# Optimization experiments

Hardware: AMD Instinct MI355X
Metric: run time of the kernel (lower is better)

## Reference

```python
import jax, jax.numpy as jnp
import numpy as np
from jax import lax

SR = 16000
N_FFT = 400
HOP = 200
N_MELS = 128
HID = 128


def _mel_fb():
    # torchaudio melscale_fbanks defaults: htk scale, norm=None, f_min=0, f_max=sr/2
    all_freqs = np.linspace(0.0, SR / 2, N_FFT // 2 + 1)  # (201,)
    hz2mel = lambda f: 2595.0 * np.log10(1.0 + f / 700.0)
    mel2hz = lambda m: 700.0 * (10.0 ** (m / 2595.0) - 1.0)
    m_pts = np.linspace(hz2mel(0.0), hz2mel(SR / 2), N_MELS + 2)
    f_pts = mel2hz(m_pts)  # (130,)
    f_diff = np.diff(f_pts)  # (129,)
    slopes = f_pts[None, :] - all_freqs[:, None]  # (201,130)
    down = -slopes[:, :-2] / f_diff[:-1]
    up = slopes[:, 2:] / f_diff[1:]
    fb = np.maximum(0.0, np.minimum(down, up))  # (201,128)
    return jnp.asarray(fb, dtype=jnp.float32)

MEL_FB = _mel_fb()
HANN = jnp.asarray(np.hanning(N_FFT + 1)[:-1], dtype=jnp.float32)  # periodic hann(400)


def mel_spectrogram(x):
    # x: (B, T) waveform -> (B, n_mels, frames), power=2 mel spectrogram
    pad = N_FFT // 2
    xp = jnp.pad(x, ((0, 0), (pad, pad)), mode='reflect')
    n_frames = 1 + (xp.shape[1] - N_FFT) // HOP  # 81 for T=16000
    idx = jnp.arange(n_frames)[:, None] * HOP + jnp.arange(N_FFT)[None, :]
    frames = xp[:, idx] * HANN  # (B, frames, 400)
    spec = jnp.fft.rfft(frames, axis=-1)  # (B, frames, 201)
    power = jnp.abs(spec) ** 2
    mel = power @ MEL_FB  # (B, frames, 128)
    return jnp.transpose(mel, (0, 2, 1))  # (B, 128, frames)


def lstm_layer(x, W, U, b):
    # x: (B, T, F); gate order i, f, g, o (matches torch slicing)
    B = x.shape[0]
    h0 = jnp.zeros((B, HID), x.dtype)
    c0 = jnp.zeros((B, HID), x.dtype)

    def step(carry, x_t):
        h, c = carry
        gates = x_t @ W + h @ U + b  # (B, 4H)
        i = jax.nn.sigmoid(gates[:, :HID])
        f = jax.nn.sigmoid(gates[:, HID:2 * HID])
        g = jnp.tanh(gates[:, 2 * HID:3 * HID])
        o = jax.nn.sigmoid(gates[:, 3 * HID:])
        c = f * c + i * g
        h = o * jnp.tanh(c)
        return (h, c), h

    _, hs = lax.scan(step, (h0, c0), jnp.transpose(x, (1, 0, 2)))  # (T, B, H)
    return jnp.transpose(hs, (1, 0, 2))  # (B, T, H)


def setup_inputs() -> dict:
    key = jax.random.key(0)
    ks = jax.random.split(key, 16)
    s = 0.05
    return {
        'x': jax.random.normal(ks[0], (1024, 16000), dtype=jnp.float32),
        'conv_w': jax.random.normal(ks[1], (128, 128, 3), dtype=jnp.float32) * s,  # (out,in,k)
        'conv_b': jax.random.normal(ks[2], (128,), dtype=jnp.float32) * s,
        'W1': jax.random.normal(ks[3], (128, 4 * HID), dtype=jnp.float32) * s,
        'U1': jax.random.normal(ks[4], (HID, 4 * HID), dtype=jnp.float32) * s,
        'b1': jax.random.normal(ks[5], (4 * HID,), dtype=jnp.float32) * s,
        'W2': jax.random.normal(ks[6], (HID, 4 * HID), dtype=jnp.float32) * s,
        'U2': jax.random.normal(ks[7], (HID, 4 * HID), dtype=jnp.float32) * s,
        'b2': jax.random.normal(ks[8], (4 * HID,), dtype=jnp.float32) * s,
        'fc1_w': jax.random.normal(ks[9], (128, 128), dtype=jnp.float32) * s,  # (in,out)
        'fc1_b': jax.random.normal(ks[10], (128,), dtype=jnp.float32) * s,
        'proj_w': jax.random.normal(ks[11], (128, 35), dtype=jnp.float32) * s,  # (in,out)
        'proj_b': jax.random.normal(ks[12], (35,), dtype=jnp.float32) * s,
    }


def reference(x, conv_w, conv_b, W1, U1, b1, W2, U2, b2, fc1_w, fc1_b, proj_w, proj_b):
    # MelSpectrogram -> Conv1d(128,128,3) -> permute -> LSTM x2 -> fc1 -> mean(time) -> proj
    spec = mel_spectrogram(x)  # (B, 128, 81)
    conv = lax.conv_general_dilated(
        spec, conv_w, window_strides=(1,), padding='VALID',
        dimension_numbers=('NCH', 'OIH', 'NCH')) + conv_b[None, :, None]  # (B,128,79)
    h = jnp.transpose(conv, (0, 2, 1))  # (B, 79, 128)
    h = lstm_layer(h, W1, U1, b1)
    h = lstm_layer(h, W2, U2, b2)
    h = h @ fc1_w + fc1_b  # (B, 79, 128)
    h = jnp.mean(h, axis=1)  # (B, 128)
    return h @ proj_w + proj_b  # (B, 35)
```

## Files before the change

kernel.cpp:

```cpp
#include <hip/hip_runtime.h>
#include <math.h>

#define PI_D 3.14159265358979323846

#define BATCH   1024
#define TLEN    16000
#define NFFT    400
#define HOP     200
#define NFRAME  81
#define NBIN    201
#define NMEL    128
#define HID     128
#define TSTEPS  79
#define GATES   512

#define KDFT    416
#define NDFT    512
#define SINOFF  256
#define KPOW    224
#define KCONV   384
#define NCHUNK  2
#define CHROWS  (BATCH*NFRAME/NCHUNK)

static inline size_t al512(size_t v){ return (v + 511) & ~((size_t)511); }

__device__ __forceinline__ unsigned short bf_rne(float f){
    unsigned u = __float_as_uint(f);
    u += 0x7FFF + ((u >> 16) & 1);
    return (unsigned short)(u >> 16);
}
__device__ __forceinline__ void bf_split(float f, unsigned short& h, unsigned short& l){
    h = bf_rne(f);
    float hf = __uint_as_float(((unsigned)h) << 16);
    l = bf_rne(f - hf);
}
__device__ __forceinline__ void bf_split_fast(float f, unsigned short& h, unsigned short& l){
    unsigned u = __float_as_uint(f);
    h = (unsigned short)(u >> 16);
    float hf = __uint_as_float(u & 0xFFFF0000u);
    l = (unsigned short)(__float_as_uint(f - hf) >> 16);
}

__device__ __forceinline__ int kswz(int n, int k){
    return (k & ~31) | (((((k >> 3) & 3) ^ ((n >> 1) & 3))) << 3) | (k & 7);
}

typedef short bf16x8 __attribute__((ext_vector_type(8)));
typedef float f32x4  __attribute__((ext_vector_type(4)));
typedef unsigned short us8 __attribute__((ext_vector_type(8)));
typedef unsigned short us4 __attribute__((ext_vector_type(4)));
typedef _Float16 f16x8 __attribute__((ext_vector_type(8)));

__device__ __forceinline__ void gld16(const unsigned short* g, unsigned short* l){
    __builtin_amdgcn_global_load_lds(
        (const __attribute__((address_space(1))) unsigned int*)g,
        (__attribute__((address_space(3))) unsigned int*)l, 16, 0, 0);
}

__global__ void setup_dft_t(unsigned short* __restrict__ th, unsigned short* __restrict__ tl){
    int idx = blockIdx.x*256 + threadIdx.x;
    if (idx >= NDFT*KDFT) return;
    int n = idx / KDFT, k = idx % KDFT;
    double v = 0.0;
    if (k < 400) {
        double w = 0.5 - 0.5*cos(2.0*PI_D*(double)k/400.0);
        if (n < NBIN)                              v = w * cos(2.0*PI_D*(double)((k*n)%400)/400.0);
        else if (n >= SINOFF && n < SINOFF + NBIN) v = w * sin(2.0*PI_D*(double)((k*(n-SINOFF))%400)/400.0);
    }
    unsigned short h, l; bf_split((float)v, h, l);
    int o = n*KDFT + kswz(n, k);
    th[o] = h; tl[o] = l;
}

__global__ void setup_fb_t(unsigned short* __restrict__ fh, unsigned short* __restrict__ fl){
    int idx = blockIdx.x*256 + threadIdx.x;
    if (idx >= NMEL*KPOW) return;
    int m = idx / KPOW, f = idx % KPOW;
    float v = 0.f;
    if (f < NBIN) {
        double melmax = 2595.0 * log10(1.0 + 8000.0/700.0);
        double p0 = 700.0*(pow(10.0, melmax*(double)(m  )/129.0/2595.0) - 1.0);
        double p1 = 700.0*(pow(10.0, melmax*(double)(m+1)/129.0/2595.0) - 1.0);
        double p2 = 700.0*(pow(10.0, melmax*(double)(m+2)/129.0/2595.0) - 1.0);
        double freq = 40.0 * (double)f;
        double dn = (freq - p0)/(p1 - p0);
        double up = (p2 - freq)/(p2 - p1);
        double t  = dn < up ? dn : up;
        if (t < 0.0) t = 0.0;
        v = (float)t;
    }
    unsigned short h, l; bf_split(v, h, l);
    int o = m*KPOW + kswz(m, f);
    fh[o] = h; fl[o] = l;
}

__global__ void setup_wc_t(unsigned short* __restrict__ wh, unsigned short* __restrict__ wl,
                           const float* __restrict__ cw){
    int idx = blockIdx.x*256 + threadIdx.x;
    if (idx >= NMEL*KCONV) return;
    int o = idx / KCONV, kk = idx % KCONV;
    int ksh = kk >> 7, i = kk & 127;
    unsigned short h, l; bf_split(cw[o*384 + i*3 + ksh], h, l);
    int p = o*KCONV + kswz(o, kk);
    wh[p] = h; wl[p] = l;
}

__global__ void setup_w_t(unsigned short* __restrict__ wh, unsigned short* __restrict__ wl,
                          const float* __restrict__ w){
    int idx = blockIdx.x*256 + threadIdx.x;
    if (idx >= GATES*HID) return;
    int c = idx / HID, i = idx % HID;
    unsigned short h, l; bf_split(w[(size_t)i*GATES + c], h, l);
    int p = c*HID + kswz(c, i);
    wh[p] = h; wl[p] = l;
}

__global__ void setup_comb(float* __restrict__ cwm, float* __restrict__ cb,
                           const float* __restrict__ fc1w, const float* __restrict__ fc1b,
                           const float* __restrict__ projw, const float* __restrict__ projb){
    int idx = blockIdx.x*256 + threadIdx.x;
    if (idx < 128*64) {
        int i = idx / 64, o = idx % 64;
        float v = 0.f;
        if (o < 35) {
            double s = 0.0;
            for (int m = 0; m < 128; m++) s += (double)fc1w[i*128+m] * (double)projw[m*35+o];
            v = (float)s;
        }
        cwm[idx] = v;
    } else if (idx < 128*64 + 64) {
        int o = idx - 128*64;
        float v = 0.f;
        if (o < 35) {
            double s = (double)projb[o];
            for (int m = 0; m < 128; m++) s += (double)fc1b[m] * (double)projw[m*35+o];
            v = (float)s;
        }
        cb[o] = v;
    }
}

__global__ void setup_uf(_Float16* __restrict__ uf, const float* __restrict__ u){
    int idx = blockIdx.x*256 + threadIdx.x;
    if (idx >= 65536) return;
    int j    = idx & 7;
    int lane = (idx >> 3) & 63;
    int nt   = (idx >> 9) & 3;
    int ks   = (idx >> 11) & 3;
    int w    = (idx >> 13) & 7;
    int k = ks*32 + (lane >> 4)*8 + j;
    int c = w*64 + nt*16 + (lane & 15);
    uf[idx] = (_Float16)u[(size_t)k*GATES + c];
}

enum AMode { A_NORMAL=0, A_FRAMES=1, A_POWER=2, A_CONV3=3 };

template<int AMODE, bool BIAS, int NT, bool WIDE>
__global__ __launch_bounds__(256)
void mgemm_k(const float* __restrict__ A,
             const unsigned short* __restrict__ BTh, const unsigned short* __restrict__ BTl,
             const float* __restrict__ bias, float* __restrict__ C,
             int Ksteps, int lda, int kstride, int ldc,
             const float* __restrict__ aux, int rowbase)
{
    constexpr int BM = WIDE ? 64 : 128;
    constexpr int BN = WIDE ? 256 : 128;
    constexpr int AP = BM / 32;
    __shared__ unsigned short Ash[2][BM][32], Asl[2][BM][32];
    __shared__ unsigned short Bsh[2][BN][32], Bsl[2][BN][32];

    const int nwg = gridDim.x;
    const int qq = nwg >> 3, rmd = nwg & 7;
    const int xcd = blockIdx.x & 7, loc = blockIdx.x >> 3;
    const int swz = (xcd < rmd ? xcd*(qq+1) : rmd*(qq+1) + (xcd - rmd)*qq) + loc;
    constexpr int LGNT = (NT == 4) ? 2 : (NT == 2) ? 1 : 0;
    const int m0 = (swz >> LGNT) * BM;
    const int n0 = (swz & (NT-1)) * BN;

    const int tid = threadIdx.x;
    const int lane = tid & 63, w = tid >> 6;
    const int wr = WIDE ? 0 : (w >> 1) * 64;
    const int wc = WIDE ? w * 64 : (w & 1) * 64;
    const int l15 = lane & 15;
    const int swf = ((lane & 15) >> 1) & 3;
    const int pos = (((lane >> 4) ^ swf) << 3);

    const int sr  = tid >> 3;
    const int wcol = (((((tid & 7) >> 1)) ^ ((tid >> 4) & 3)) << 3) + ((tid & 1) << 2);

    float va0[AP*4], vb0[AP*4], va1[AP*4], vb1[AP*4];

    auto issue_loads = [&](float (&va)[AP*4], float (&vb)[AP*4], int ksn){
        const int k0n = ksn * 32;
        #pragma unroll
        for (int p = 0; p < AP; p++) {
            const int row = p*32 + sr;
            const int kk = k0n + (tid & 7)*4;
            if constexpr (AMODE == A_NORMAL) {
                *(float4*)&va[p*4] = *(const float4*)(A + (size_t)(m0+row)*lda + kk);
            } else if constexpr (AMODE == A_POWER) {
                const float* src = A + (size_t)(m0+row)*lda + kk;
                *(float4*)&va[p*4] = *(const float4*)(src);
                *(float4*)&vb[p*4] = *(const float4*)(src + SINOFF);
            } else if constexpr (AMODE == A_FRAMES) {
                const int rr = rowbase + m0 + row;
                const int b = rr / NFRAME, f = rr - b*NFRAME;
                const float* xb = aux + (size_t)b * TLEN;
                const int q0 = f*HOP + kk - 200;
                if (q0 >= 0 && q0 + 3 < TLEN) {
                    *(float4*)&va[p*4] = *(const float4*)(xb + q0);
                } else {
                    #pragma unroll
                    for (int j = 0; j < 4; j++) {
                        int q = q0 + j;
                        if (q < 0) q = -q;
                        else if (q >= TLEN) q = 2*TLEN - 2 - q;
                        va[p*4+j] = xb[q];
                    }
                }
            } else {
                const int rr = m0 + row;
                const int b = rr / TSTEPS, t = rr - b*TSTEPS;
                const int ksh = kk >> 7, i = kk & 127;
                *(float4*)&va[p*4] = *(const float4*)(aux + ((size_t)(b*NFRAME + t + ksh)*NMEL + i));
            }
        }
        (void)vb;
    };
    auto write_stage = [&](float (&va)[AP*4], float (&vb)[AP*4], int wb){
        #pragma unroll
        for (int p = 0; p < AP; p++) {
            const int row = p*32 + sr;
            us4 hv, lv;
            #pragma unroll
            for (int j = 0; j < 4; j++) {
                float f = va[p*4+j];
                if constexpr (AMODE == A_POWER) f = f*f + vb[p*4+j]*vb[p*4+j];
                unsigned short h, l; bf_split_fast(f, h, l);
                hv[j] = h; lv[j] = l;
            }
            *(us4*)&Ash[wb][row][wcol] = hv;
            *(us4*)&Asl[wb][row][wcol] = lv;
        }
        (void)vb;
    };
    auto dma_b = [&](int wb, int ksn){
        const int k0n = ksn * 32;
        if constexpr (WIDE) {
            #pragma unroll
            for (int p = 0; p < 4; p++) {
                const int row = w*64 + p*16;
                const size_t o = (size_t)(n0 + row + (lane >> 2))*kstride + k0n + (lane & 3)*8;
                gld16(BTh + o, &Bsh[wb][row][0]);
                gld16(BTl + o, &Bsl[wb][row][0]);
            }
        } else {
            #pragma unroll
            for (int p = 0; p < 2; p++) {
                const int row = p*64 + w*16;
                const size_t o = (size_t)(n0 + row + (lane >> 2))*kstride + k0n + (lane & 3)*8;
                gld16(BTh + o, &Bsh[wb][row][0]);
                gld16(BTl + o, &Bsl[wb][row][0]);
            }
        }
    };

    f32x4 acc[4][4] = {};

    issue_loads(va1, vb1, 0);
    dma_b(0, 0);
    write_stage(va1, vb1, 0);
    issue_loads(va0, vb0, 1);
    __syncthreads();

    auto iter = [&](int ks, float (&vac)[AP*4], float (&vbc)[AP*4],
                    float (&vao)[AP*4], float (&vbo)[AP*4], int bufc){
        const bool pf1 = (ks + 1 < Ksteps);
        const bool pf2 = (ks + 2 < Ksteps);
        if (pf2) issue_loads(vao, vbo, ks + 2);
        if (pf1) dma_b(bufc ^ 1, ks + 1);

        bf16x8 ah[4], al[4];
        #pragma unroll
        for (int mt = 0; mt < 4; mt++) {
            ah[mt] = *(const bf16x8*)&Ash[bufc][wr + mt*16 + l15][pos];
            al[mt] = *(const bf16x8*)&Asl[bufc][wr + mt*16 + l15][pos];
        }
        #pragma unroll
        for (int nt = 0; nt < 4; nt++) {
            const int nr = wc + nt*16 + l15;
            bf16x8 bh = *(const bf16x8*)&Bsh[bufc][nr][pos];
            bf16x8 bl = *(const bf16x8*)&Bsl[bufc][nr][pos];
            #pragma unroll
            for (int mt = 0; mt < 4; mt++) {
                acc[mt][nt] = __builtin_amdgcn_mfma_f32_16x16x32_bf16(ah[mt], bh, acc[mt][nt], 0, 0, 0);
                acc[mt][nt] = __builtin_amdgcn_mfma_f32_16x16x32_bf16(ah[mt], bl, acc[mt][nt], 0, 0, 0);
                acc[mt][nt] = __builtin_amdgcn_mfma_f32_16x16x32_bf16(al[mt], bh, acc[mt][nt], 0, 0, 0);
            }
        }

        if (pf1) {
            write_stage(vac, vbc, bufc ^ 1);
            __syncthreads();
        }
    };

    for (int ks = 0; ks < Ksteps; ks += 2) {
        iter(ks, va0, vb0, va1, vb1, 0);
        if (ks + 1 < Ksteps) iter(ks + 1, va1, vb1, va0, vb0, 1);
    }

    const int quad = lane >> 4;
    #pragma unroll
    for (int nt = 0; nt < 4; nt++) {
        const int col = n0 + wc + (nt << 4) + l15;
        float b = 0.f;
        if constexpr (BIAS) b = bias[col];
        #pragma unroll
        for (int mt = 0; mt < 4; mt++) {
            #pragma unroll
            for (int r = 0; r < 4; r++) {
                const int row = m0 + wr + (mt << 4) + quad*4 + r;
                C[(size_t)row*ldc + col] = acc[mt][nt][r] + b;
            }
        }
    }
}

__global__ __launch_bounds__(256)
void gemm_small(const float* __restrict__ A, const float* __restrict__ Bm,
                const float* __restrict__ bias, float* __restrict__ C,
                int M, int N, int K, int lda, int ldb, int ldc)
{
    __shared__ float As[16][64+4];
    __shared__ float Bs[16][64];
    const int tid = threadIdx.x;
    const int tx = tid & 15, ty = tid >> 4;
    const int m0 = blockIdx.x * 64;
    float acc[4][4] = {{0,0,0,0},{0,0,0,0},{0,0,0,0},{0,0,0,0}};
    const int am = tid >> 2, ak = (tid & 3) * 4;
    const int bk = tid >> 4, bn = (tid & 15) * 4;
    for (int k0 = 0; k0 < K; k0 += 16) {
        float4 av = *(const float4*)(A + (size_t)(m0+am)*lda + k0 + ak);
        As[ak+0][am]=av.x; As[ak+1][am]=av.y; As[ak+2][am]=av.z; As[ak+3][am]=av.w;
        *(float4*)&Bs[bk][bn] = *(const float4*)(Bm + (size_t)(k0+bk)*ldb + bn);
        __syncthreads();
        #pragma unroll
        for (int k = 0; k < 16; k++) {
            float4 a = *(const float4*)&As[k][ty*4];
            float4 b = *(const float4*)&Bs[k][tx*4];
            #pragma unroll
            for (int i = 0; i < 4; i++) {
                float av_ = ((const float*)&a)[i];
                acc[i][0] = fmaf(av_, b.x, acc[i][0]);
                acc[i][1] = fmaf(av_, b.y, acc[i][1]);
                acc[i][2] = fmaf(av_, b.z, acc[i][2]);
                acc[i][3] = fmaf(av_, b.w, acc[i][3]);
            }
        }
        __syncthreads();
    }
    #pragma unroll
    for (int ir = 0; ir < 4; ir++) {
        const int row = m0 + ty*4 + ir;
        #pragma unroll
        for (int jc = 0; jc < 4; jc++) {
            const int col = tx*4 + jc;
            if (col < N) C[(size_t)row*ldc + col] = acc[ir][jc] + bias[col];
        }
    }
}

__device__ __forceinline__ float sigm_f(float x){ return 1.f/(1.f + __expf(-x)); }
__device__ __forceinline__ float tanh_f(float x){ float e = __expf(2.f*x); return 1.f - 2.f/(e + 1.f); }

#define LROWS 4
#define LTHREADS 512
#define HPAD 136

__global__ __launch_bounds__(LTHREADS, 2)
void lstm_k(const float* __restrict__ X, const _Float16* __restrict__ Uf, float* __restrict__ H)
{
    __shared__ _Float16 hsA[16*HPAD];
    __shared__ float gs[GATES*5];
    const int tid = threadIdx.x;
    const int b0 = blockIdx.x * LROWS;
    const int lane = tid & 63, w = tid >> 6;
    const int m16 = lane & 15, quad = lane >> 4;
    const int r = tid >> 7;
    const int j = tid & 127;

    f32x4 bfr[4][4];
    #pragma unroll
    for (int ks = 0; ks < 4; ks++)
        #pragma unroll
        for (int nt = 0; nt < 4; nt++) {
            bfr[ks][nt] = *(const f32x4*)(Uf + ((((w*4 + ks)*4 + nt)*64 + lane) << 3));
            asm volatile("" : "+v"(bfr[ks][nt]));
        }

    for (int i = tid; i < 16*HPAD; i += LTHREADS) hsA[i] = (_Float16)0.f;
    float cst = 0.f;
    const float* xb = X + ((size_t)(b0 + r)*TSTEPS)*GATES + j;
    __syncthreads();

    float xi = xb[0], xf = xb[128], xg = xb[256], xo = xb[384];

    for (int t = 0; t < TSTEPS; t++) {
        float xi_n = 0.f, xf_n = 0.f, xg_n = 0.f, xo_n = 0.f;
        if (t + 1 < TSTEPS) {
            const float* xp = xb + (size_t)(t + 1)*GATES;
            xi_n = xp[0]; xf_n = xp[128]; xg_n = xp[256]; xo_n = xp[384];
        }

        f16x8 ah[4];
        #pragma unroll
        for (int ks = 0; ks < 4; ks++)
            ah[ks] = *(const f16x8*)&hsA[m16*HPAD + ks*32 + quad*8];

        f32x4 acc[4] = {{0,0,0,0},{0,0,0,0},{0,0,0,0},{0,0,0,0}};
        #pragma unroll
        for (int ks = 0; ks < 4; ks++)
            #pragma unroll
            for (int nt = 0; nt < 4; nt++)
                acc[nt] = __builtin_amdgcn_mfma_f32_16x16x32_f16(
                    ah[ks], __builtin_bit_cast(f16x8, bfr[ks][nt]), acc[nt], 0, 0, 0);

        if (quad == 0) {
            #pragma unroll
            for (int nt = 0; nt < 4; nt++) {
                const int c = w*64 + nt*16 + m16;
                #pragma unroll
                for (int rr = 0; rr < 4; rr++) gs[c*5 + rr] = acc[nt][rr];
            }
        }
        __syncthreads();

        {
            const float gi = gs[(      j)*5 + r] + xi;
            const float gf = gs[(128 + j)*5 + r] + xf;
            const float gg = gs[(256 + j)*5 + r] + xg;
            const float go = gs[(384 + j)*5 + r] + xo;
            const float cn = sigm_f(gf)*cst + sigm_f(gi)*tanh_f(gg);
            cst = cn;
            const float hn = sigm_f(go)*tanh_f(cn);
            H[((size_t)(b0 + r)*TSTEPS + t)*HID + j] = hn;
            hsA[r*HPAD + j] = (_Float16)hn;
        }
        __syncthreads();

        xi = xi_n; xf = xf_n; xg = xg_n; xo = xo_n;
    }
}

__global__ void mean_k(const float* __restrict__ H, float* __restrict__ Mh){
    const int idx = blockIdx.x*256 + threadIdx.x;
    if (idx >= BATCH*HID) return;
    const int b = idx >> 7, j = idx & 127;
    const float* p = H + (size_t)b*TSTEPS*HID + j;
    float s = 0.f;
    for (int t = 0; t < TSTEPS; t++) s += p[(size_t)t*HID];
    Mh[idx] = s * (1.0f/(float)TSTEPS);
}

extern "C" void kernel_launch(void* const* d_in, const int* in_sizes, int n_in,
                              void* d_out, int out_size, void* d_ws, size_t ws_size,
                              hipStream_t stream)
{
    const float* x      = (const float*)d_in[0];
    const float* conv_w = (const float*)d_in[1];
    const float* conv_b = (const float*)d_in[2];
    const float* W1     = (const float*)d_in[3];
    const float* U1     = (const float*)d_in[4];
    const float* b1     = (const float*)d_in[5];
    const float* W2     = (const float*)d_in[6];
    const float* U2     = (const float*)d_in[7];
    const float* b2     = (const float*)d_in[8];
    const float* fc1_w  = (const float*)d_in[9];
    const float* fc1_b  = (const float*)d_in[10];
    const float* proj_w = (const float*)d_in[11];
    const float* proj_b = (const float*)d_in[12];
    float* out = (float*)d_out;

    char* ws = (char*)d_ws;
    size_t off = 0;
    unsigned short* Tth = (unsigned short*)(ws + off); off = al512(off + (size_t)NDFT*KDFT*2);
    unsigned short* Ttl = (unsigned short*)(ws + off); off = al512(off + (size_t)NDFT*KDFT*2);
    unsigned short* fbh = (unsigned short*)(ws + off); off = al512(off + (size_t)NMEL*KPOW*2);
    unsigned short* fbl = (unsigned short*)(ws + off); off = al512(off + (size_t)NMEL*KPOW*2);
    unsigned short* wch = (unsigned short*)(ws + off); off = al512(off + (size_t)NMEL*KCONV*2);
    unsigned short* wcl = (unsigned short*)(ws + off); off = al512(off + (size_t)NMEL*KCONV*2);
    unsigned short* w1h = (unsigned short*)(ws + off); off = al512(off + (size_t)GATES*HID*2);
    unsigned short* w1l = (unsigned short*)(ws + off); off = al512(off + (size_t)GATES*HID*2);
    unsigned short* w2h = (unsigned short*)(ws + off); off = al512(off + (size_t)GATES*HID*2);
    unsigned short* w2l = (unsigned short*)(ws + off); off = al512(off + (size_t)GATES*HID*2);
    float* Cw   = (float*)(ws + off); off = al512(off + (size_t)128*64*4);
    float* Cb   = (float*)(ws + off); off = al512(off + (size_t)64*4);
    float* Mh   = (float*)(ws + off); off = al512(off + (size_t)BATCH*HID*4);
    _Float16* Uf1 = (_Float16*)(ws + off); off = al512(off + (size_t)65536*2);
    _Float16* Uf2 = (_Float16*)(ws + off); off = al512(off + (size_t)65536*2);
    float* MEL  = (float*)(ws + off); off = al512(off + (size_t)BATCH*NFRAME*NMEL*4);
    float* CONV = (float*)(ws + off); off = al512(off + (size_t)BATCH*TSTEPS*NMEL*4);
    float* X    = (float*)(ws + off); off = al512(off + (size_t)BATCH*TSTEPS*GATES*4);
    float* DFT = X;
    float* H1  = MEL;
    float* H2  = CONV;
    (void)ws_size; (void)out_size; (void)n_in; (void)in_sizes;

    setup_dft_t<<<(NDFT*KDFT + 255)/256, 256, 0, stream>>>(Tth, Ttl);
    setup_fb_t <<<(NMEL*KPOW + 255)/256, 256, 0, stream>>>(fbh, fbl);
    setup_wc_t <<<(NMEL*KCONV + 255)/256, 256, 0, stream>>>(wch, wcl, conv_w);
    setup_w_t  <<<(GATES*HID + 255)/256, 256, 0, stream>>>(w1h, w1l, W1);
    setup_w_t  <<<(GATES*HID + 255)/256, 256, 0, stream>>>(w2h, w2l, W2);
    setup_comb <<<(128*64 + 64 + 255)/256, 256, 0, stream>>>(Cw, Cb, fc1_w, fc1_b, proj_w, proj_b);
    setup_uf   <<<65536/256, 256, 0, stream>>>(Uf1, U1);
    setup_uf   <<<65536/256, 256, 0, stream>>>(Uf2, U2);

    for (int ch = 0; ch < NCHUNK; ch++) {
        const int rowbase = ch * CHROWS;
        mgemm_k<A_FRAMES,false,2,true><<<(CHROWS/64)*2, 256, 0, stream>>>(
            nullptr, Tth, Ttl, nullptr, DFT, KDFT/32, 0, KDFT, NDFT, x, rowbase);
        mgemm_k<A_POWER,false,1,false><<<CHROWS/128, 256, 0, stream>>>(
            DFT, fbh, fbl, nullptr, MEL + (size_t)rowbase*NMEL, KPOW/32, NDFT, KPOW, NMEL, nullptr, 0);
    }

    mgemm_k<A_CONV3,true,1,false><<<BATCH*TSTEPS/128, 256, 0, stream>>>(
        nullptr, wch, wcl, conv_b, CONV, KCONV/32, 0, KCONV, NMEL, MEL, 0);

    mgemm_k<A_NORMAL,true,2,true><<<(BATCH*TSTEPS/64)*2, 256, 0, stream>>>(
        CONV, w1h, w1l, b1, X, HID/32, NMEL, HID, GATES, nullptr, 0);
    lstm_k<<<BATCH/LROWS, LTHREADS, 0, stream>>>(X, Uf1, H1);

    mgemm_k<A_NORMAL,true,2,true><<<(BATCH*TSTEPS/64)*2, 256, 0, stream>>>(
        H1, w2h, w2l, b2, X, HID/32, HID, HID, GATES, nullptr, 0);
    lstm_k<<<BATCH/LROWS, LTHREADS, 0, stream>>>(X, Uf2, H2);

    mean_k<<<(BATCH*HID + 255)/256, 256, 0, stream>>>(H2, Mh);
    gemm_small<<<BATCH/64, 256, 0, stream>>>(Mh, Cw, Cb, out, BATCH, 35, HID, HID, 64, 35);
}
```

Measured before the change: 666.1 us.

## Replace LSTM step barriers with LDS-only waits, spread gate writes, deepen prefetch

```diff
diff --git a/kernel.cpp b/kernel.cpp
--- a/kernel.cpp
+++ b/kernel.cpp
@@ -55,6 +55,13 @@
     __builtin_amdgcn_global_load_lds(
         (const __attribute__((address_space(1))) unsigned int*)g,
         (__attribute__((address_space(3))) unsigned int*)l, 16, 0, 0);
+}
+
+__device__ __forceinline__ void barrier_lds(){
+    __builtin_amdgcn_sched_barrier(0);
+    asm volatile("s_waitcnt lgkmcnt(0)" ::: "memory");
+    __builtin_amdgcn_s_barrier();
+    __builtin_amdgcn_sched_barrier(0);
 }
 
 __global__ void setup_dft_t(unsigned short* __restrict__ th, unsigned short* __restrict__ tl){
@@ -404,13 +411,14 @@
     const float* xb = X + ((size_t)(b0 + r)*TSTEPS)*GATES + j;
     __syncthreads();
 
-    float xi = xb[0], xf = xb[128], xg = xb[256], xo = xb[384];
+    float xi  = xb[0],     xf  = xb[128],     xg  = xb[256],     xo  = xb[384];
+    float xi1 = xb[GATES], xf1 = xb[GATES+128], xg1 = xb[GATES+256], xo1 = xb[GATES+384];
 
     for (int t = 0; t < TSTEPS; t++) {
-        float xi_n = 0.f, xf_n = 0.f, xg_n = 0.f, xo_n = 0.f;
-        if (t + 1 < TSTEPS) {
-            const float* xp = xb + (size_t)(t + 1)*GATES;
-            xi_n = xp[0]; xf_n = xp[128]; xg_n = xp[256]; xo_n = xp[384];
+        float xi2 = 0.f, xf2 = 0.f, xg2 = 0.f, xo2 = 0.f;
+        if (t + 2 < TSTEPS) {
+            const float* xp = xb + (size_t)(t + 2)*GATES;
+            xi2 = xp[0]; xf2 = xp[128]; xg2 = xp[256]; xo2 = xp[384];
         }
 
         f16x8 ah[4];
@@ -426,15 +434,17 @@
                 acc[nt] = __builtin_amdgcn_mfma_f32_16x16x32_f16(
                     ah[ks], __builtin_bit_cast(f16x8, bfr[ks][nt]), acc[nt], 0, 0, 0);
 
-        if (quad == 0) {
-            #pragma unroll
-            for (int nt = 0; nt < 4; nt++) {
-                const int c = w*64 + nt*16 + m16;
-                #pragma unroll
-                for (int rr = 0; rr < 4; rr++) gs[c*5 + rr] = acc[nt][rr];
-            }
-        }
-        __syncthreads();
+        {
+            const f32x4 s0 = (quad & 1) ? acc[1] : acc[0];
+            const f32x4 s1 = (quad & 1) ? acc[3] : acc[2];
+            const f32x4 av = (quad & 2) ? s1 : s0;
+            const int c = w*64 + quad*16 + m16;
+            gs[c*5 + 0] = av[0];
+            gs[c*5 + 1] = av[1];
+            gs[c*5 + 2] = av[2];
+            gs[c*5 + 3] = av[3];
+        }
+        barrier_lds();
 
         {
             const float gi = gs[(      j)*5 + r] + xi;
@@ -445,11 +455,16 @@
             cst = cn;
             const float hn = sigm_f(go)*tanh_f(cn);
             H[((size_t)(b0 + r)*TSTEPS + t)*HID + j] = hn;
-            hsA[r*HPAD + j] = (_Float16)hn;
-        }
-        __syncthreads();
-
-        xi = xi_n; xf = xf_n; xg = xg_n; xo = xo_n;
+            const _Float16 hh = (_Float16)hn;
+            hsA[(r     )*HPAD + j] = hh;
+            hsA[(r +  4)*HPAD + j] = hh;
+            hsA[(r +  8)*HPAD + j] = hh;
+            hsA[(r + 12)*HPAD + j] = hh;
+        }
+        barrier_lds();
+
+        xi = xi1; xf = xf1; xg = xg1; xo = xo1;
+        xi1 = xi2; xf1 = xf2; xg1 = xg2; xo1 = xo2;
     }
 }
 
```

After: 671.3 us. About the same (+0.8%).
